# Kernel optimization log

Hardware: AMD Instinct MI355X
Metric: run time of the kernel (lower is better)

The kernel has to match this reference:

```python
import jax, jax.numpy as jnp
import numpy as np

H = 1024          # hidden_size
M = 512           # moe_intermediate_size
E = 16            # n_routed_experts
TOP_K = 4         # num_experts_per_tok
N_GROUP = 4
TOPK_GROUP = 2
SCALE = 2.5       # routed_scaling_factor
B, S = 2, 1024


def setup_inputs() -> dict:
    key = jax.random.key(0)
    ks = jax.random.split(key, 9)
    sc_h = 1.0 / np.sqrt(H)
    sc_m = 1.0 / np.sqrt(M)
    return {
        "hidden_states": jax.random.normal(ks[0], (B, S, H), jnp.float32),
        "gate_kernel": jax.random.normal(ks[1], (H, E), jnp.float32) * sc_h,
        "gate_bias": jax.random.normal(ks[2], (E,), jnp.float32) * 0.01,
        "w_gate": jax.random.normal(ks[3], (E, H, M), jnp.float32) * sc_h,
        "w_up": jax.random.normal(ks[4], (E, H, M), jnp.float32) * sc_h,
        "w_down": jax.random.normal(ks[5], (E, M, H), jnp.float32) * sc_m,
        "sw_gate": jax.random.normal(ks[6], (H, 2 * M), jnp.float32) * sc_h,
        "sw_up": jax.random.normal(ks[7], (H, 2 * M), jnp.float32) * sc_h,
        "sw_down": jax.random.normal(ks[8], (2 * M, H), jnp.float32) * (1.0 / np.sqrt(2 * M)),
    }


def _gate(x2d, gate_kernel, gate_bias):
    # x2d: [N, H]
    n = x2d.shape[0]
    logits = jnp.dot(x2d.astype(jnp.float32), gate_kernel.astype(jnp.float32))  # [N, E]
    scores = jax.nn.sigmoid(logits)
    scores_for_choice = scores + gate_bias  # noaux_tc correction bias
    # group-limited top-k: sum of top-2 scores per group
    group_scores = scores_for_choice.reshape(n, N_GROUP, E // N_GROUP)
    top2 = jax.lax.top_k(group_scores, k=2)[0]
    group_sum = jnp.sum(top2, axis=-1)                       # [N, G]
    group_idx = jax.lax.top_k(group_sum, k=TOPK_GROUP)[1]    # [N, topk_group]
    group_mask = jnp.zeros_like(group_sum).at[jnp.arange(n)[:, None], group_idx].set(1.0)
    score_mask = jnp.repeat(group_mask[:, :, None], E // N_GROUP, axis=2).reshape(n, E)
    masked_scores = jnp.where(score_mask > 0, scores_for_choice, 0.0)
    topk_weight, topk_idx = jax.lax.top_k(masked_scores, k=TOP_K)
    # norm_topk_prob
    topk_weight = topk_weight / (jnp.sum(topk_weight, axis=-1, keepdims=True) + 1e-20)
    topk_weight = topk_weight * SCALE
    return topk_idx, topk_weight


def reference(hidden_states, gate_kernel, gate_bias, w_gate, w_up, w_down,
              sw_gate, sw_up, sw_down):
    orig_shape = hidden_states.shape
    x = hidden_states.reshape(-1, orig_shape[-1])  # [N, H]
    topk_idx, topk_weight = _gate(x, gate_kernel, gate_bias)
    # combine weight per (token, expert): sum_k (topk_idx==e) * topk_weight
    onehot = (topk_idx[:, :, None] == jnp.arange(E)[None, None, :]).astype(topk_weight.dtype)
    combine = jnp.einsum('nke,nk->ne', onehot, topk_weight)  # [N, E]
    # dense per-expert MLP (faithful to moe_infer which runs every expert)
    g = jnp.einsum('nh,ehm->enm', x, w_gate)   # [E, N, M]
    u = jnp.einsum('nh,ehm->enm', x, w_up)
    inter = jax.nn.silu(g) * u
    y_e = jnp.einsum('enm,emh->enh', inter, w_down)          # [E, N, H]
    y = jnp.einsum('ne,enh->nh', combine, y_e)               # [N, H]
    # shared-expert path
    shared = jnp.dot(jax.nn.silu(jnp.dot(x, sw_gate)) * jnp.dot(x, sw_up), sw_down)
    return (y + shared).reshape(orig_shape)
```

## Files before the change

### kernel.cpp

```cpp
#include <hip/hip_runtime.h>
#include <hip/hip_bf16.h>
#include <cstdint>

#define HID    1024
#define MID    512
#define NEXP   16
#define NTOKS  2048
#define TOPKE  4
#define RSCALE 2.5f
#define CSTR   16

typedef __attribute__((ext_vector_type(8))) short  bf16x8;
typedef __attribute__((ext_vector_type(8))) ushort u16x8;
typedef __attribute__((ext_vector_type(4))) float  f32x4;

__device__ __forceinline__ ushort f2bf(float f){
  unsigned u = __float_as_uint(f);
  u += 0x7fffu + ((u >> 16) & 1u);
  return (ushort)(u >> 16);
}
__device__ __forceinline__ float bf2f(ushort h){ return __uint_as_float(((unsigned)h) << 16); }

#define GLD16(g, l) __builtin_amdgcn_global_load_lds( \
    (const __attribute__((address_space(1))) unsigned int*)(g), \
    (__attribute__((address_space(3))) unsigned int*)(l), 16, 0, 0)

__device__ __forceinline__ void tr_tile(const float* __restrict__ in,
                                        ushort* __restrict__ out,
                                        int K, int N, int kb, int nb,
                                        float* __restrict__ T)
{
  const int t  = threadIdx.x;
  const int r  = t >> 4;
  const int c4 = (t & 15) * 4;
  #pragma unroll
  for (int i = 0; i < 4; ++i){
    f32x4 v = *reinterpret_cast<const f32x4*>(in + (size_t)(kb + r + i*16) * N + nb + c4);
    #pragma unroll
    for (int j = 0; j < 4; ++j)
      T[(r + i*16) * 65 + c4 + j] = v[j];
  }
  __syncthreads();
  const int n = t >> 2;
  const int q = t & 3;
  u16x8 o0, o1;
  #pragma unroll
  for (int j = 0; j < 8; ++j) o0[j] = f2bf(T[(q*16 + j) * 65 + n]);
  #pragma unroll
  for (int j = 0; j < 8; ++j) o1[j] = f2bf(T[(q*16 + 8 + j) * 65 + n]);
  ushort* op = out + (size_t)(nb + n) * K + kb + q * 16;
  *reinterpret_cast<u16x8*>(op)     = o0;
  *reinterpret_cast<u16x8*>(op + 8) = o1;
}

__global__ __launch_bounds__(256) void k_pre0(
    const float* __restrict__ x, ushort* __restrict__ xb,
    const float* __restrict__ gk, const float* __restrict__ gb,
    const float* __restrict__ swg, const float* __restrict__ swu,
    const float* __restrict__ swd,
    ushort* __restrict__ swgT, ushort* __restrict__ swuT,
    ushort* __restrict__ swdT,
    int* __restrict__ counts, int* __restrict__ tidx, float* __restrict__ tw)
{
  __shared__ float T[64 * 65];
  __shared__ float sc[16][16];
  __shared__ int lcnt[NEXP];
  const int z = blockIdx.z;
  const int bid = blockIdx.y * 8 + blockIdx.x;

  if (z < 6){
    const int m = z >> 1;
    const float* in = (m == 0) ? swg : (m == 1) ? swu : swd;
    ushort* out     = (m == 0) ? swgT : (m == 1) ? swuT : swdT;
    tr_tile(in, out, 1024, 1024, blockIdx.y * 64, (z & 1) * 512 + blockIdx.x * 64, T);
    return;
  }
  if (z == 6){
    #pragma unroll
    for (int j = 0; j < 8; ++j){
      int i = bid * 2048 + j * 256 + threadIdx.x;
      f32x4 a = *reinterpret_cast<const f32x4*>(x + (size_t)i*8);
      f32x4 b = *reinterpret_cast<const f32x4*>(x + (size_t)i*8 + 4);
      u16x8 o;
      o[0]=f2bf(a[0]); o[1]=f2bf(a[1]); o[2]=f2bf(a[2]); o[3]=f2bf(a[3]);
      o[4]=f2bf(b[0]); o[5]=f2bf(b[1]); o[6]=f2bf(b[2]); o[7]=f2bf(b[3]);
      *reinterpret_cast<u16x8*>(xb + (size_t)i*8) = o;
    }
    return;
  }
  {
    const int tid = threadIdx.x;
    const int tl  = tid >> 4;
    const int e   = tid & 15;
    const int t   = bid * 16 + tl;
    float acc = 0.f;
    const float* xr = x + (size_t)t * HID;
    for (int h = 0; h < HID; h += 4){
      f32x4 xv = *reinterpret_cast<const f32x4*>(xr + h);
      acc += xv[0] * gk[(h+0)*NEXP + e];
      acc += xv[1] * gk[(h+1)*NEXP + e];
      acc += xv[2] * gk[(h+2)*NEXP + e];
      acc += xv[3] * gk[(h+3)*NEXP + e];
    }
    sc[tl][e] = 1.f / (1.f + expf(-acc)) + gb[e];
    if (tid < NEXP) lcnt[tid] = 0;
    __syncthreads();
    if (tid < 16){
      const int tt = bid * 16 + tid;
      float s4[NEXP];
      #pragma unroll
      for (int i = 0; i < NEXP; ++i) s4[i] = sc[tid][i];
      float gs[4];
      #pragma unroll
      for (int g = 0; g < 4; ++g){
        float m1 = -1e30f, m2 = -1e30f;
        #pragma unroll
        for (int j = 0; j < 4; ++j){
          float v = s4[g*4+j];
          if (v > m1){ m2 = m1; m1 = v; } else if (v > m2){ m2 = v; }
        }
        gs[g] = m1 + m2;
      }
      int g1 = 0;
      for (int g = 1; g < 4; ++g) if (gs[g] > gs[g1]) g1 = g;
      int g2 = -1;
      for (int g = 0; g < 4; ++g){
        if (g == g1) continue;
        if (g2 < 0 || gs[g] > gs[g2]) g2 = g;
      }
      float ms[NEXP];
      #pragma unroll
      for (int i = 0; i < NEXP; ++i){
        int g = i >> 2;
        ms[i] = (g == g1 || g == g2) ? s4[i] : 0.0f;
      }
      bool used[NEXP];
      #pragma unroll
      for (int i = 0; i < NEXP; ++i) used[i] = false;
      int sel[TOPKE]; float val[TOPKE]; float denom = 0.f;
      #pragma unroll
      for (int k = 0; k < TOPKE; ++k){
        int be = -1; float bv = -1e30f;
        for (int i = 0; i < NEXP; ++i){
          if (used[i]) continue;
          if (ms[i] > bv){ bv = ms[i]; be = i; }
        }
        used[be] = true; sel[k] = be; val[k] = bv; denom += bv;
      }
      float inv = RSCALE / (denom + 1e-20f);
      #pragma unroll
      for (int k = 0; k < TOPKE; ++k){
        tidx[tt*TOPKE + k] = sel[k];
        tw  [tt*TOPKE + k] = val[k] * inv;
        atomicAdd(&lcnt[sel[k]], 1);
      }
    }
    __syncthreads();
    if (tid < NEXP && lcnt[tid]) atomicAdd(&counts[tid * CSTR], lcnt[tid]);
  }
}

__global__ __launch_bounds__(256) void k_place(const int* __restrict__ tidx,
                                               const float* __restrict__ tw,
                                               const int* __restrict__ counts,
                                               int* __restrict__ cursor,
                                               int* __restrict__ tlist,
                                               float* __restrict__ wlist,
                                               int* __restrict__ pos)
{
  __shared__ int lcnt[NEXP];
  __shared__ int lbase[NEXP];
  __shared__ int soff[NEXP];
  const int tid = threadIdx.x;
  const int t = blockIdx.x * 256 + tid;
  if (tid < NEXP){
    lcnt[tid] = 0;
    int s = 0;
    for (int i = 0; i < tid; ++i) s += counts[i * CSTR];
    soff[tid] = s;
  }
  __syncthreads();
  int sel[TOPKE]; float w4[TOPKE]; int ls[TOPKE];
  #pragma unroll
  for (int k = 0; k < TOPKE; ++k){
    sel[k] = tidx[t*TOPKE + k];
    w4[k]  = tw[t*TOPKE + k];
    ls[k]  = atomicAdd(&lcnt[sel[k]], 1);
  }
  __syncthreads();
  if (tid < NEXP) lbase[tid] = atomicAdd(&cursor[tid * CSTR], lcnt[tid]);
  __syncthreads();
  #pragma unroll
  for (int k = 0; k < TOPKE; ++k){
    int p = soff[sel[k]] + lbase[sel[k]] + ls[k];
    tlist[p] = t;
    wlist[p] = w4[k];
    pos[t*TOPKE + k] = p;
  }
}

__global__ __launch_bounds__(256) void k_mmS(
    const ushort* __restrict__ xb, ushort* __restrict__ i_s,
    const ushort* __restrict__ swgT, const ushort* __restrict__ swuT,
    const float* __restrict__ wg, const float* __restrict__ wu,
    const float* __restrict__ wd,
    ushort* __restrict__ wgT, ushort* __restrict__ wuT,
    ushort* __restrict__ wdT)
{
  __shared__ __align__(16) ushort Sh[16384];
  const int z = blockIdx.z;
  if (z >= 34){
    const int e = z - 34;
    tr_tile(wd + (size_t)e * MID * HID, wdT + (size_t)e * MID * HID,
            512, 1024, blockIdx.x * 64, blockIdx.y * 64, (float*)Sh);
    return;
  }
  if (z >= 2){
    const bool isU = (z >= 18);
    const int e = isU ? (z - 18) : (z - 2);
    const float* in = (isU ? wu : wg) + (size_t)e * HID * MID;
    ushort* out     = (isU ? wuT : wgT) + (size_t)e * HID * MID;
    tr_tile(in, out, 1024, 512, blockIdx.y * 64, blockIdx.x * 64, (float*)Sh);
    return;
  }

  const int mbase   = blockIdx.y * 128;
  const int colBase = z * 512 + blockIdx.x * 64;

  const int tid = threadIdx.x;
  const int l   = tid & 63;
  const int w   = tid >> 6;
  const int wm  = w >> 1;
  const int wn  = w & 1;

  const int rl     = l >> 3;
  const int srcOff = 8 * ((l & 7) ^ rl);

  const ushort* srcP[8];
  #pragma unroll
  for (int j = 0; j < 8; ++j){
    int g = w * 8 + j;
    const ushort* p;
    if (g < 16){
      p = xb + (size_t)(mbase + g * 8 + rl) * HID;
    } else if (g < 24){
      p = swgT + (size_t)(colBase + (g - 16) * 8 + rl) * HID;
    } else {
      p = swuT + (size_t)(colBase + (g - 24) * 8 + rl) * HID;
    }
    srcP[j] = p + srcOff;
  }

  f32x4 accg[4][2], accu[4][2];
  #pragma unroll
  for (int i = 0; i < 4; ++i)
    #pragma unroll
    for (int j = 0; j < 2; ++j){
      accg[i][j] = (f32x4){0.f,0.f,0.f,0.f};
      accu[i][j] = (f32x4){0.f,0.f,0.f,0.f};
    }

  const int fr  = l & 15;
  const int ko  = l >> 4;
  const int swz = (fr & 7) << 4;

  for (int kt = 0; kt < 16; ++kt){
    const int ke = kt * 64;
    #pragma unroll
    for (int j = 0; j < 8; ++j)
      GLD16(srcP[j] + ke, (ushort*)Sh + (w*8 + j) * 512 + l * 8);
    __syncthreads();
    #pragma unroll
    for (int ks = 0; ks < 2; ++ks){
      const int co = ks * 64 + ko * 16;
      bf16x8 af[4], bg[2], bu[2];
      #pragma unroll
      for (int mf = 0; mf < 4; ++mf)
        af[mf] = *reinterpret_cast<const bf16x8*>(
            (const char*)Sh + (wm*64 + mf*16 + fr) * 128 + (co ^ swz));
      #pragma unroll
      for (int nf = 0; nf < 2; ++nf){
        int cc = wn*32 + nf*16 + fr;
        bg[nf] = *reinterpret_cast<const bf16x8*>(
            (const char*)Sh + 16384 + cc * 128 + (co ^ swz));
        bu[nf] = *reinterpret_cast<const bf16x8*>(
            (const char*)Sh + 24576 + cc * 128 + (co ^ swz));
      }
      #pragma unroll
      for (int mf = 0; mf < 4; ++mf)
        #pragma unroll
        for (int nf = 0; nf < 2; ++nf){
          accg[mf][nf] = __builtin_amdgcn_mfma_f32_16x16x32_bf16(af[mf], bg[nf], accg[mf][nf], 0, 0, 0);
          accu[mf][nf] = __builtin_amdgcn_mfma_f32_16x16x32_bf16(af[mf], bu[nf], accu[mf][nf], 0, 0, 0);
        }
    }
    __syncthreads();
  }

  const int ccol = l & 15;
  const int crow = (l >> 4) * 4;
  #pragma unroll
  for (int mf = 0; mf < 4; ++mf){
    #pragma unroll
    for (int r_ = 0; r_ < 4; ++r_){
      const int row = wm*64 + mf*16 + crow + r_ + mbase;
      #pragma unroll
      for (int nf = 0; nf < 2; ++nf){
        int col = colBase + wn*32 + nf*16 + ccol;
        float g = accg[mf][nf][r_];
        float u = accu[mf][nf][r_];
        float s = g / (1.f + expf(-g));
        i_s[(size_t)row * 1024 + col] = f2bf(s * u);
      }
    }
  }
}

__global__ __launch_bounds__(256) void k_mmR(
    const ushort* __restrict__ xb, ushort* __restrict__ i_r,
    const ushort* __restrict__ wgT, const ushort* __restrict__ wuT,
    const ushort* __restrict__ i_s, const ushort* __restrict__ swdT,
    ushort* __restrict__ y_s,
    const int* __restrict__ counts, const int* __restrict__ tlist)
{
  __shared__ __align__(16) ushort Sh[16384];
  const int z = blockIdx.z;

  const int tid = threadIdx.x;
  const int l   = tid & 63;
  const int w   = tid >> 6;
  const int rl     = l >> 3;
  const int srcOff = 8 * ((l & 7) ^ rl);
  const int fr  = l & 15;
  const int ko  = l >> 4;
  const int swz = (fr & 7) << 4;
  const int ccol = l & 15;
  const int crow = (l >> 4) * 4;

  if (z == 16){
    if (blockIdx.y >= 16) return;
    const int wm  = w >> 1;
    const int wn  = w & 1;
    const int mbase = blockIdx.y * 128;
    const int nbase = blockIdx.x * 128;
    const ushort* srcP[8];
    #pragma unroll
    for (int j = 0; j < 8; ++j){
      int g = w * 8 + j;
      const ushort* p;
      if (g < 16) p = i_s + (size_t)(mbase + g * 8 + rl) * HID;
      else        p = swdT + (size_t)(nbase + (g - 16) * 8 + rl) * HID;
      srcP[j] = p + srcOff;
    }
    f32x4 acc[4][4];
    #pragma unroll
    for (int i = 0; i < 4; ++i)
      #pragma unroll
      for (int j = 0; j < 4; ++j)
        acc[i][j] = (f32x4){0.f,0.f,0.f,0.f};
    for (int kt = 0; kt < 16; ++kt){
      const int ke = kt * 64;
      #pragma unroll
      for (int j = 0; j < 8; ++j)
        GLD16(srcP[j] + ke, (ushort*)Sh + (w*8 + j) * 512 + l * 8);
      __syncthreads();
      #pragma unroll
      for (int ks = 0; ks < 2; ++ks){
        const int co = ks * 64 + ko * 16;
        bf16x8 af[4], bf[4];
        #pragma unroll
        for (int mf = 0; mf < 4; ++mf)
          af[mf] = *reinterpret_cast<const bf16x8*>(
              (const char*)Sh + (wm*64 + mf*16 + fr) * 128 + (co ^ swz));
        #pragma unroll
        for (int nf = 0; nf < 4; ++nf)
          bf[nf] = *reinterpret_cast<const bf16x8*>(
              (const char*)Sh + 16384 + (wn*64 + nf*16 + fr) * 128 + (co ^ swz));
        #pragma unroll
        for (int mf = 0; mf < 4; ++mf)
          #pragma unroll
          for (int nf = 0; nf < 4; ++nf)
            acc[mf][nf] = __builtin_amdgcn_mfma_f32_16x16x32_bf16(af[mf], bf[nf], acc[mf][nf], 0, 0, 0);
      }
      __syncthreads();
    }
    #pragma unroll
    for (int mf = 0; mf < 4; ++mf)
      #pragma unroll
      for (int r_ = 0; r_ < 4; ++r_){
        const int row = wm*64 + mf*16 + crow + r_ + mbase;
        #pragma unroll
        for (int nf = 0; nf < 4; ++nf){
          int col = nbase + wn*64 + nf*16 + ccol;
          y_s[(size_t)row * HID + col] = f2bf(acc[mf][nf][r_]);
        }
      }
    return;
  }

  const int e = z;
  const int mbase = blockIdx.y * 64;
  const int cnt = counts[e * CSTR];
  if (mbase >= cnt) return;
  int aoff = 0;
  for (int i = 0; i < e; ++i) aoff += counts[i * CSTR];

  const int colBase = blockIdx.x * 64;
  const ushort* Bg = wgT + (size_t)e * MID * HID;
  const ushort* Bu = wuT + (size_t)e * MID * HID;

  const int wm  = w >> 1;
  const int wn  = w & 1;

  const ushort* srcP[6];
  #pragma unroll
  for (int j = 0; j < 6; ++j){
    int g = w * 6 + j;
    const ushort* p;
    if (g < 8){
      int ar = mbase + g * 8 + rl;
      int s = aoff + (ar < cnt ? ar : cnt - 1);
      p = xb + (size_t)tlist[s] * HID;
    } else if (g < 16){
      p = Bg + (size_t)(colBase + (g - 8) * 8 + rl) * HID;
    } else {
      p = Bu + (size_t)(colBase + (g - 16) * 8 + rl) * HID;
    }
    srcP[j] = p + srcOff;
  }

  f32x4 accg[2][2], accu[2][2];
  #pragma unroll
  for (int i = 0; i < 2; ++i)
    #pragma unroll
    for (int j = 0; j < 2; ++j){
      accg[i][j] = (f32x4){0.f,0.f,0.f,0.f};
      accu[i][j] = (f32x4){0.f,0.f,0.f,0.f};
    }

  for (int kt = 0; kt < 16; ++kt){
    const int ke = kt * 64;
    #pragma unroll
    for (int j = 0; j < 6; ++j)
      GLD16(srcP[j] + ke, (ushort*)Sh + (w*6 + j) * 512 + l * 8);
    __syncthreads();
    #pragma unroll
    for (int ks = 0; ks < 2; ++ks){
      const int co = ks * 64 + ko * 16;
      bf16x8 af[2], bg[2], bu[2];
      #pragma unroll
      for (int mf = 0; mf < 2; ++mf)
        af[mf] = *reinterpret_cast<const bf16x8*>(
            (const char*)Sh + (wm*32 + mf*16 + fr) * 128 + (co ^ swz));
      #pragma unroll
      for (int nf = 0; nf < 2; ++nf){
        int cc = wn*32 + nf*16 + fr;
        bg[nf] = *reinterpret_cast<const bf16x8*>(
            (const char*)Sh + 8192 + cc * 128 + (co ^ swz));
        bu[nf] = *reinterpret_cast<const bf16x8*>(
            (const char*)Sh + 16384 + cc * 128 + (co ^ swz));
      }
      #pragma unroll
      for (int mf = 0; mf < 2; ++mf)
        #pragma unroll
        for (int nf = 0; nf < 2; ++nf){
          accg[mf][nf] = __builtin_amdgcn_mfma_f32_16x16x32_bf16(af[mf], bg[nf], accg[mf][nf], 0, 0, 0);
          accu[mf][nf] = __builtin_amdgcn_mfma_f32_16x16x32_bf16(af[mf], bu[nf], accu[mf][nf], 0, 0, 0);
        }
    }
    __syncthreads();
  }

  #pragma unroll
  for (int mf = 0; mf < 2; ++mf){
    #pragma unroll
    for (int r_ = 0; r_ < 4; ++r_){
      const int arel = wm*32 + mf*16 + crow + r_ + mbase;
      if (arel >= cnt) continue;
      size_t row = (size_t)(aoff + arel);
      #pragma unroll
      for (int nf = 0; nf < 2; ++nf){
        int col = colBase + wn*32 + nf*16 + ccol;
        float g = accg[mf][nf][r_];
        float u = accu[mf][nf][r_];
        float s = g / (1.f + expf(-g));
        i_r[row * 512 + col] = f2bf(s * u);
      }
    }
  }
}

__global__ __launch_bounds__(256) void k_mm1(
    const ushort* __restrict__ i_r, const ushort* __restrict__ wdT,
    ushort* __restrict__ y_r,
    const int* __restrict__ counts, const float* __restrict__ wlist)
{
  const int e = blockIdx.z;
  const int mbase = blockIdx.y * 64;
  const int nbase = blockIdx.x * 128;
  const int cnt = counts[e * CSTR];
  if (mbase >= cnt) return;
  int aoff = 0;
  for (int i = 0; i < e; ++i) aoff += counts[i * CSTR];
  const ushort* B = wdT + (size_t)e * HID * MID;

  __shared__ __align__(16) ushort Sh[12288];

  const int tid = threadIdx.x;
  const int l   = tid & 63;
  const int w   = tid >> 6;
  const int wm  = w >> 1;
  const int wn  = w & 1;
  const int rl     = l >> 3;
  const int srcOff = 8 * ((l & 7) ^ rl);

  const ushort* srcP[6];
  #pragma unroll
  for (int j = 0; j < 6; ++j){
    int g = w * 6 + j;
    const ushort* p;
    if (g < 8){
      int ar = mbase + g * 8 + rl;
      int s = aoff + (ar < cnt ? ar : cnt - 1);
      p = i_r + (size_t)s * MID;
    } else {
      p = B + (size_t)(nbase + (g - 8) * 8 + rl) * MID;
    }
    srcP[j] = p + srcOff;
  }

  f32x4 acc[2][4];
  #pragma unroll
  for (int i = 0; i < 2; ++i)
    #pragma unroll
    for (int j = 0; j < 4; ++j)
      acc[i][j] = (f32x4){0.f,0.f,0.f,0.f};

  const int fr  = l & 15;
  const int ko  = l >> 4;
  const int swz = (fr & 7) << 4;

  for (int kt = 0; kt < 8; ++kt){
    const int ke = kt * 64;
    #pragma unroll
    for (int j = 0; j < 6; ++j)
      GLD16(srcP[j] + ke, (ushort*)Sh + (w*6 + j) * 512 + l * 8);
    __syncthreads();
    #pragma unroll
    for (int ks = 0; ks < 2; ++ks){
      const int co = ks * 64 + ko * 16;
      bf16x8 af[2], bf[4];
      #pragma unroll
      for (int mf = 0; mf < 2; ++mf)
        af[mf] = *reinterpret_cast<const bf16x8*>(
            (const char*)Sh + (wm*32 + mf*16 + fr) * 128 + (co ^ swz));
      #pragma unroll
      for (int nf = 0; nf < 4; ++nf)
        bf[nf] = *reinterpret_cast<const bf16x8*>(
            (const char*)Sh + 8192 + (wn*64 + nf*16 + fr) * 128 + (co ^ swz));
      #pragma unroll
      for (int mf = 0; mf < 2; ++mf)
        #pragma unroll
        for (int nf = 0; nf < 4; ++nf)
          acc[mf][nf] = __builtin_amdgcn_mfma_f32_16x16x32_bf16(af[mf], bf[nf], acc[mf][nf], 0, 0, 0);
    }
    __syncthreads();
  }

  const int ccol = l & 15;
  const int crow = (l >> 4) * 4;
  #pragma unroll
  for (int mf = 0; mf < 2; ++mf){
    #pragma unroll
    for (int r_ = 0; r_ < 4; ++r_){
      const int arel = wm*32 + mf*16 + crow + r_ + mbase;
      if (arel >= cnt) continue;
      int s = aoff + arel;
      float wgt = wlist[s];
      #pragma unroll
      for (int nf = 0; nf < 4; ++nf){
        int col = nbase + wn*64 + nf*16 + ccol;
        y_r[(size_t)s * HID + col] = f2bf(wgt * acc[mf][nf][r_]);
      }
    }
  }
}

__global__ __launch_bounds__(256) void k_comb(const ushort* __restrict__ y_s,
                                              const ushort* __restrict__ y_r,
                                              const int* __restrict__ pos,
                                              float* __restrict__ out)
{
  const int t  = blockIdx.x * 2 + (threadIdx.x >> 7);
  const int c8 = (threadIdx.x & 127) * 8;
  const int* pp = pos + t * TOPKE;
  u16x8 vs = *reinterpret_cast<const u16x8*>(y_s + (size_t)t * HID + c8);
  float s[8];
  #pragma unroll
  for (int j = 0; j < 8; ++j) s[j] = bf2f(vs[j]);
  #pragma unroll
  for (int k = 0; k < TOPKE; ++k){
    int p = pp[k];
    u16x8 vr = *reinterpret_cast<const u16x8*>(y_r + (size_t)p * HID + c8);
    #pragma unroll
    for (int j = 0; j < 8; ++j) s[j] += bf2f(vr[j]);
  }
  f32x4 o0 = (f32x4){s[0],s[1],s[2],s[3]};
  f32x4 o1 = (f32x4){s[4],s[5],s[6],s[7]};
  *reinterpret_cast<f32x4*>(out + (size_t)t * HID + c8)     = o0;
  *reinterpret_cast<f32x4*>(out + (size_t)t * HID + c8 + 4) = o1;
}

extern "C" void kernel_launch(void* const* d_in, const int* in_sizes, int n_in,
                              void* d_out, int out_size, void* d_ws, size_t ws_size,
                              hipStream_t stream)
{
  const float* x   = (const float*)d_in[0];
  const float* gk  = (const float*)d_in[1];
  const float* gb  = (const float*)d_in[2];
  const float* wg  = (const float*)d_in[3];
  const float* wu  = (const float*)d_in[4];
  const float* wd  = (const float*)d_in[5];
  const float* swg = (const float*)d_in[6];
  const float* swu = (const float*)d_in[7];
  const float* swd = (const float*)d_in[8];
  float* out = (float*)d_out;
  char* ws = (char*)d_ws;

  const size_t MB = 1ull << 20;
  int*    counts = (int*)(ws + 0);
  int*    cursor = (int*)(ws + 2048);
  int*    tidx   = (int*)(ws + 8192);
  float*  tw     = (float*)(ws + 49152);
  int*    tlist  = (int*)(ws + 90112);
  float*  wlist  = (float*)(ws + 131072);
  int*    pos    = (int*)(ws + 163840);
  ushort* xb     = (ushort*)(ws + 1*MB);
  ushort* swgT   = (ushort*)(ws + 5*MB);
  ushort* swuT   = (ushort*)(ws + 7*MB);
  ushort* swdT   = (ushort*)(ws + 9*MB);
  ushort* wgT    = (ushort*)(ws + 11*MB);
  ushort* wuT    = (ushort*)(ws + 27*MB);
  ushort* wdT    = (ushort*)(ws + 43*MB);
  ushort* i_s    = (ushort*)(ws + 59*MB);
  ushort* i_r    = (ushort*)(ws + 63*MB);
  ushort* y_s    = (ushort*)(ws + 71*MB);
  ushort* y_r    = (ushort*)(ws + 11*MB);

  hipMemsetAsync(ws, 0, 4096, stream);
  k_pre0<<<dim3(8,16,8), 256, 0, stream>>>(x, xb, gk, gb, swg, swu, swd,
                                           swgT, swuT, swdT, counts, tidx, tw);
  k_place<<<NTOKS/256, 256, 0, stream>>>(tidx, tw, counts, cursor, tlist, wlist, pos);

  k_mmS<<<dim3(8,16,50), 256, 0, stream>>>(xb, i_s, swgT, swuT, wg, wu, wd,
                                           wgT, wuT, wdT);
  k_mmR<<<dim3(8,32,17), 256, 0, stream>>>(xb, i_r, wgT, wuT, i_s, swdT, y_s,
                                           counts, tlist);
  k_mm1<<<dim3(8,32,16), 256, 0, stream>>>(i_r, wdT, y_r, counts, wlist);
  k_comb<<<NTOKS/2, 256, 0, stream>>>(y_s, y_r, pos, out);
}
```

Measured before the change: 151.2 us.

## Move shared-expert down projection from routed gate/up kernel into down-proj kernel

The shared-expert down projection (i_s x swdT) moves out of k_mmR, where it ran as 128x128 tiles in an extra z-slice, and into k_mm1 as a 17th z-slice using k_mm1's 64x128 tiles with K=1024. k_mmR shrinks its LDS to 12288 elements and no longer carries the large-tile branch, which may improve occupancy and register use. The shared down-projection now runs as 256 smaller tiles alongside the routed down projections, which is meant to balance work across the two launches. In exchange, the smaller tiles give less data reuse for that GEMM.

```diff
diff --git a/kernel.cpp b/kernel.cpp
--- a/kernel.cpp
+++ b/kernel.cpp
@@ -319,12 +319,9 @@
 __global__ __launch_bounds__(256) void k_mmR(
     const ushort* __restrict__ xb, ushort* __restrict__ i_r,
     const ushort* __restrict__ wgT, const ushort* __restrict__ wuT,
-    const ushort* __restrict__ i_s, const ushort* __restrict__ swdT,
-    ushort* __restrict__ y_s,
     const int* __restrict__ counts, const int* __restrict__ tlist)
 {
-  __shared__ __align__(16) ushort Sh[16384];
-  const int z = blockIdx.z;
+  __shared__ __align__(16) ushort Sh[12288];
 
   const int tid = threadIdx.x;
   const int l   = tid & 63;
@@ -337,68 +334,7 @@
   const int ccol = l & 15;
   const int crow = (l >> 4) * 4;
 
-  if (z == 16){
-    if (blockIdx.y >= 16) return;
-    const int wm  = w >> 1;
-    const int wn  = w & 1;
-    const int mbase = blockIdx.y * 128;
-    const int nbase = blockIdx.x * 128;
-    const ushort* srcP[8];
-    #pragma unroll
-    for (int j = 0; j < 8; ++j){
-      int g = w * 8 + j;
-      const ushort* p;
-      if (g < 16) p = i_s + (size_t)(mbase + g * 8 + rl) * HID;
-      else        p = swdT + (size_t)(nbase + (g - 16) * 8 + rl) * HID;
-      srcP[j] = p + srcOff;
-    }
-    f32x4 acc[4][4];
-    #pragma unroll
-    for (int i = 0; i < 4; ++i)
-      #pragma unroll
-      for (int j = 0; j < 4; ++j)
-        acc[i][j] = (f32x4){0.f,0.f,0.f,0.f};
-    for (int kt = 0; kt < 16; ++kt){
-      const int ke = kt * 64;
-      #pragma unroll
-      for (int j = 0; j < 8; ++j)
-        GLD16(srcP[j] + ke, (ushort*)Sh + (w*8 + j) * 512 + l * 8);
-      __syncthreads();
-      #pragma unroll
-      for (int ks = 0; ks < 2; ++ks){
-        const int co = ks * 64 + ko * 16;
-        bf16x8 af[4], bf[4];
-        #pragma unroll
-        for (int mf = 0; mf < 4; ++mf)
-          af[mf] = *reinterpret_cast<const bf16x8*>(
-              (const char*)Sh + (wm*64 + mf*16 + fr) * 128 + (co ^ swz));
-        #pragma unroll
-        for (int nf = 0; nf < 4; ++nf)
-          bf[nf] = *reinterpret_cast<const bf16x8*>(
-              (const char*)Sh + 16384 + (wn*64 + nf*16 + fr) * 128 + (co ^ swz));
-        #pragma unroll
-        for (int mf = 0; mf < 4; ++mf)
-          #pragma unroll
-          for (int nf = 0; nf < 4; ++nf)
-            acc[mf][nf] = __builtin_amdgcn_mfma_f32_16x16x32_bf16(af[mf], bf[nf], acc[mf][nf], 0, 0, 0);
-      }
-      __syncthreads();
-    }
-    #pragma unroll
-    for (int mf = 0; mf < 4; ++mf)
-      #pragma unroll
-      for (int r_ = 0; r_ < 4; ++r_){
-        const int row = wm*64 + mf*16 + crow + r_ + mbase;
-        #pragma unroll
-        for (int nf = 0; nf < 4; ++nf){
-          int col = nbase + wn*64 + nf*16 + ccol;
-          y_s[(size_t)row * HID + col] = f2bf(acc[mf][nf][r_]);
-        }
-      }
-    return;
-  }
-
-  const int e = z;
+  const int e = blockIdx.z;
   const int mbase = blockIdx.y * 64;
   const int cnt = counts[e * CSTR];
   if (mbase >= cnt) return;
@@ -493,19 +429,13 @@
 __global__ __launch_bounds__(256) void k_mm1(
     const ushort* __restrict__ i_r, const ushort* __restrict__ wdT,
     ushort* __restrict__ y_r,
+    const ushort* __restrict__ i_s, const ushort* __restrict__ swdT,
+    ushort* __restrict__ y_s,
     const int* __restrict__ counts, const float* __restrict__ wlist)
 {
-  const int e = blockIdx.z;
-  const int mbase = blockIdx.y * 64;
-  const int nbase = blockIdx.x * 128;
-  const int cnt = counts[e * CSTR];
-  if (mbase >= cnt) return;
-  int aoff = 0;
-  for (int i = 0; i < e; ++i) aoff += counts[i * CSTR];
-  const ushort* B = wdT + (size_t)e * HID * MID;
-
   __shared__ __align__(16) ushort Sh[12288];
 
+  const int z = blockIdx.z;
   const int tid = threadIdx.x;
   const int l   = tid & 63;
   const int w   = tid >> 6;
@@ -513,6 +443,27 @@
   const int wn  = w & 1;
   const int rl     = l >> 3;
   const int srcOff = 8 * ((l & 7) ^ rl);
+  const int fr  = l & 15;
+  const int ko  = l >> 4;
+  const int swz = (fr & 7) << 4;
+  const int ccol = l & 15;
+  const int crow = (l >> 4) * 4;
+
+  const bool shared_dn = (z == 16);
+  const int mbase = blockIdx.y * 64;
+  const int nbase = blockIdx.x * 128;
+
+  int e = 0, cnt = NTOKS, aoff = 0, Kd = HID;
+  const ushort* A; const ushort* B;
+  if (shared_dn){
+    A = i_s; B = swdT; Kd = HID;
+  } else {
+    e = z;
+    cnt = counts[e * CSTR];
+    if (mbase >= cnt) return;
+    for (int i = 0; i < e; ++i) aoff += counts[i * CSTR];
+    A = i_r; B = wdT + (size_t)e * HID * MID; Kd = MID;
+  }
 
   const ushort* srcP[6];
   #pragma unroll
@@ -521,10 +472,14 @@
     const ushort* p;
     if (g < 8){
       int ar = mbase + g * 8 + rl;
-      int s = aoff + (ar < cnt ? ar : cnt - 1);
-      p = i_r + (size_t)s * MID;
+      if (shared_dn){
+        p = A + (size_t)ar * Kd;
+      } else {
+        int s = aoff + (ar < cnt ? ar : cnt - 1);
+        p = A + (size_t)s * Kd;
+      }
     } else {
-      p = B + (size_t)(nbase + (g - 8) * 8 + rl) * MID;
+      p = B + (size_t)(nbase + (g - 8) * 8 + rl) * Kd;
     }
     srcP[j] = p + srcOff;
   }
@@ -536,11 +491,8 @@
     for (int j = 0; j < 4; ++j)
       acc[i][j] = (f32x4){0.f,0.f,0.f,0.f};
 
-  const int fr  = l & 15;
-  const int ko  = l >> 4;
-  const int swz = (fr & 7) << 4;
-
-  for (int kt = 0; kt < 8; ++kt){
+  const int nk = Kd >> 6;
+  for (int kt = 0; kt < nk; ++kt){
     const int ke = kt * 64;
     #pragma unroll
     for (int j = 0; j < 6; ++j)
@@ -567,20 +519,26 @@
     __syncthreads();
   }
 
-  const int ccol = l & 15;
-  const int crow = (l >> 4) * 4;
   #pragma unroll
   for (int mf = 0; mf < 2; ++mf){
     #pragma unroll
     for (int r_ = 0; r_ < 4; ++r_){
       const int arel = wm*32 + mf*16 + crow + r_ + mbase;
-      if (arel >= cnt) continue;
-      int s = aoff + arel;
-      float wgt = wlist[s];
-      #pragma unroll
-      for (int nf = 0; nf < 4; ++nf){
-        int col = nbase + wn*64 + nf*16 + ccol;
-        y_r[(size_t)s * HID + col] = f2bf(wgt * acc[mf][nf][r_]);
+      if (shared_dn){
+        #pragma unroll
+        for (int nf = 0; nf < 4; ++nf){
+          int col = nbase + wn*64 + nf*16 + ccol;
+          y_s[(size_t)arel * HID + col] = f2bf(acc[mf][nf][r_]);
+        }
+      } else {
+        if (arel >= cnt) continue;
+        int s = aoff + arel;
+        float wgt = wlist[s];
+        #pragma unroll
+        for (int nf = 0; nf < 4; ++nf){
+          int col = nbase + wn*64 + nf*16 + ccol;
+          y_r[(size_t)s * HID + col] = f2bf(wgt * acc[mf][nf][r_]);
+        }
       }
     }
   }
@@ -654,8 +612,8 @@
 
   k_mmS<<<dim3(8,16,50), 256, 0, stream>>>(xb, i_s, swgT, swuT, wg, wu, wd,
                                            wgT, wuT, wdT);
-  k_mmR<<<dim3(8,32,17), 256, 0, stream>>>(xb, i_r, wgT, wuT, i_s, swdT, y_s,
-                                           counts, tlist);
-  k_mm1<<<dim3(8,32,16), 256, 0, stream>>>(i_r, wdT, y_r, counts, wlist);
+  k_mmR<<<dim3(8,32,16), 256, 0, stream>>>(xb, i_r, wgT, wuT, counts, tlist);
+  k_mm1<<<dim3(8,32,17), 256, 0, stream>>>(i_r, wdT, y_r, i_s, swdT, y_s,
+                                           counts, wlist);
   k_comb<<<NTOKS/2, 256, 0, stream>>>(y_s, y_r, pos, out);
 }
```

Result: slower. 156.4 us (+3.4%).
